# Optimization experiments

Hardware: AMD Instinct MI355X
Metric: run time of the kernel (lower is better)

Reference implementation:

```python
import jax, jax.numpy as jnp
import numpy as np

D_MODEL = 256
N_HEADS = 8
N_LEVELS = 4
N_POINTS = 4
SHAPES = np.array([[64, 64], [32, 32], [16, 16], [8, 8]], dtype=np.int32)


def setup_inputs() -> dict:
    key = jax.random.key(0)
    ks = jax.random.split(key, 10)
    Lq = int((SHAPES[:, 0] * SHAPES[:, 1]).sum())  # 5440
    N, d = 8, D_MODEL
    noff = N_HEADS * N_LEVELS * N_POINTS * 2
    nw = N_HEADS * N_LEVELS * N_POINTS
    s = 1.0 / np.sqrt(d).astype(np.float32)
    inp = {
        'query': jax.random.normal(ks[0], (N, Lq, d), jnp.float32),
        'reference_points': jax.random.uniform(ks[1], (N, Lq, N_LEVELS, 2), jnp.float32),
        'spatial_shapes': jnp.asarray(SHAPES),
        'level_start_index': jnp.asarray(np.concatenate([[0], np.cumsum(SHAPES[:, 0] * SHAPES[:, 1])[:-1]]).astype(np.int32)),
        'W_value': jax.random.normal(ks[2], (d, d), jnp.float32) * s,
        'b_value': jnp.zeros((d,), jnp.float32),
        'W_off': jax.random.normal(ks[3], (d, noff), jnp.float32) * 0.01,
        'b_off': jax.random.uniform(ks[4], (noff,), jnp.float32, minval=-0.5, maxval=0.5),
        'W_attn': jax.random.normal(ks[5], (d, nw), jnp.float32) * s,
        'b_attn': jnp.zeros((nw,), jnp.float32),
        'W_out': jax.random.normal(ks[6], (d, d), jnp.float32) * s,
        'b_out': jnp.zeros((d,), jnp.float32),
    }
    return inp


def _bilinear_sample(val_l, loc_l, H, W):
    # val_l: [N, h, H*W, dh] flattened level feature map
    # loc_l: [N, Lq, h, P, 2] normalized (x, y) in [0, 1]
    # grid_sample semantics, align_corners=False, zero padding
    N, h, HW, dh = val_l.shape
    Lq, P = loc_l.shape[1], loc_l.shape[3]
    x = loc_l[..., 0] * W - 0.5
    y = loc_l[..., 1] * H - 0.5
    x0 = jnp.floor(x)
    y0 = jnp.floor(y)
    wx = (x - x0)[..., None]  # [N, Lq, h, P, 1]
    wy = (y - y0)[..., None]
    x0i = x0.astype(jnp.int32)
    y0i = y0.astype(jnp.int32)

    def gather(yi, xi):
        valid = (xi >= 0) & (xi < W) & (yi >= 0) & (yi < H)  # [N, Lq, h, P]
        idx = jnp.clip(yi, 0, H - 1) * W + jnp.clip(xi, 0, W - 1)
        idx = idx.transpose(0, 2, 1, 3).reshape(N, h, Lq * P)  # [N, h, Lq*P]
        g = jnp.take_along_axis(val_l, jnp.broadcast_to(idx[..., None], (N, h, Lq * P, dh)), axis=2)
        g = g.reshape(N, h, Lq, P, dh)
        mask = valid.transpose(0, 2, 1, 3)[..., None].astype(val_l.dtype)
        return g * mask

    v00 = gather(y0i, x0i)
    v01 = gather(y0i, x0i + 1)
    v10 = gather(y0i + 1, x0i)
    v11 = gather(y0i + 1, x0i + 1)
    wxt = wx.transpose(0, 2, 1, 3, 4)  # [N, h, Lq, P, 1]
    wyt = wy.transpose(0, 2, 1, 3, 4)
    return (v00 * (1 - wxt) * (1 - wyt) + v01 * wxt * (1 - wyt)
            + v10 * (1 - wxt) * wyt + v11 * wxt * wyt)  # [N, h, Lq, P, dh]


def reference(query, reference_points, spatial_shapes, level_start_index,
              W_value, b_value, W_off, b_off, W_attn, b_attn, W_out, b_out):
    shapes = np.asarray(spatial_shapes)  # static level shapes
    N, Lq, d = query.shape
    h, L, P = N_HEADS, N_LEVELS, N_POINTS
    dh = d // h

    v = query @ W_value + b_value  # value_proj (source reassigns query = value_proj(query))
    off = (v @ W_off + b_off).reshape(N, Lq, h, L, P, 2)
    aw = jax.nn.softmax((v @ W_attn + b_attn).reshape(N, Lq, h, L * P), axis=-1)
    aw = aw.reshape(N, Lq, h, L, P)

    # offset_normalizer = [W_l, H_l]
    norm = jnp.asarray(np.stack([shapes[:, 1], shapes[:, 0]], -1), dtype=v.dtype)  # [L, 2]
    loc = reference_points[:, :, None, :, None, :] + off / norm[None, None, None, :, None, :]

    val = v.reshape(N, Lq, h, dh).transpose(0, 2, 1, 3)  # [N, h, Lv, dh]
    out = jnp.zeros((N, h, Lq, dh), v.dtype)
    start = 0
    for l in range(L):
        H, W = int(shapes[l, 0]), int(shapes[l, 1])
        val_l = val[:, :, start:start + H * W]
        sampled = _bilinear_sample(val_l, loc[:, :, :, l], H, W)  # [N, h, Lq, P, dh]
        w_l = aw[:, :, :, l].transpose(0, 2, 1, 3)[..., None]  # [N, h, Lq, P, 1]
        out = out + (sampled * w_l).sum(axis=3)
        start += H * W

    out = out.transpose(0, 2, 1, 3).reshape(N, Lq, d)
    return out @ W_out + b_out
```

## Files before the change

### kernel.cpp

```cpp
#include <hip/hip_runtime.h>
#include <hip/hip_bf16.h>
#include <cstdint>
#include <cstddef>

#define NB 8
#define LQ 5440
#define MROWS (NB * LQ)

typedef __attribute__((ext_vector_type(8))) _Float16       f16x8;
typedef __attribute__((ext_vector_type(4))) float          f32x4;
typedef __attribute__((ext_vector_type(8))) unsigned short ushort8_t;

__device__ __forceinline__ unsigned short f2h(float f) {
    _Float16 h = (_Float16)f;
    unsigned short u;
    __builtin_memcpy(&u, &h, 2);
    return u;
}
__device__ __forceinline__ float h2f(unsigned short u) {
    _Float16 h;
    __builtin_memcpy(&h, &u, 2);
    return (float)h;
}

__global__ __launch_bounds__(256) void prep_weights(
    const float* __restrict__ Wv, const float* __restrict__ Woff,
    const float* __restrict__ Wat, const float* __restrict__ Wo,
    unsigned short* __restrict__ WvT, unsigned short* __restrict__ WoaT,
    unsigned short* __restrict__ WoT)
{
    const int id = blockIdx.x * 256 + threadIdx.x;
    if (id < 65536) {
        const int n = id >> 8, k = id & 255;
        WvT[id] = f2h(Wv[k * 256 + n]);
    } else if (id < 65536 + 98304) {
        const int p = id - 65536;
        const int n = p >> 8, k = p & 255;
        WoaT[p] = (n < 256) ? f2h(Woff[k * 256 + n])
                            : f2h(Wat[k * 128 + (n - 256)]);
    } else {
        const int p = id - (65536 + 98304);
        const int n = p >> 8, k = p & 255;
        WoT[p] = f2h(Wo[k * 256 + n]);
    }
}

#define LDT 40

template<bool A_FP32, bool F16_OUT>
__global__ __launch_bounds__(256) void gemm_mfma(
    const void* __restrict__ Ap, const unsigned short* __restrict__ Bt,
    const float* __restrict__ bias0, const float* __restrict__ bias1,
    void* __restrict__ C0, void* __restrict__ C1,
    int cs0, int cs1, int split)
{
    __shared__ unsigned short As[128 * LDT];
    __shared__ unsigned short Bs[128 * LDT];

    const int bm = blockIdx.y * 128;
    const int bn = blockIdx.x * 128;
    const int t    = threadIdx.x;
    const int lane = t & 63;
    const int wid  = t >> 6;
    const int wm   = (wid >> 1) * 64;
    const int wn   = (wid & 1) * 64;
    const int c    = lane & 15;
    const int qq   = lane >> 4;

    const int tr = t >> 1;
    const int kh = (t & 1) * 16;

    f32x4 acc[4][4];
#pragma unroll
    for (int i = 0; i < 4; ++i)
#pragma unroll
        for (int j = 0; j < 4; ++j)
            acc[i][j] = (f32x4){0.f, 0.f, 0.f, 0.f};

    for (int k0 = 0; k0 < 256; k0 += 32) {
        if (A_FP32) {
            const float4* Af = reinterpret_cast<const float4*>(
                (const float*)Ap + (size_t)(bm + tr) * 256 + k0 + kh);
            const float4 a0 = Af[0], a1 = Af[1], a2 = Af[2], a3 = Af[3];
            ushort8_t u0, u1;
            u0[0]=f2h(a0.x); u0[1]=f2h(a0.y); u0[2]=f2h(a0.z); u0[3]=f2h(a0.w);
            u0[4]=f2h(a1.x); u0[5]=f2h(a1.y); u0[6]=f2h(a1.z); u0[7]=f2h(a1.w);
            u1[0]=f2h(a2.x); u1[1]=f2h(a2.y); u1[2]=f2h(a2.z); u1[3]=f2h(a2.w);
            u1[4]=f2h(a3.x); u1[5]=f2h(a3.y); u1[6]=f2h(a3.z); u1[7]=f2h(a3.w);
            *reinterpret_cast<ushort8_t*>(&As[tr * LDT + kh])     = u0;
            *reinterpret_cast<ushort8_t*>(&As[tr * LDT + kh + 8]) = u1;
        } else {
            const ushort8_t* Ab = reinterpret_cast<const ushort8_t*>(
                (const unsigned short*)Ap + (size_t)(bm + tr) * 256 + k0 + kh);
            *reinterpret_cast<ushort8_t*>(&As[tr * LDT + kh])     = Ab[0];
            *reinterpret_cast<ushort8_t*>(&As[tr * LDT + kh + 8]) = Ab[1];
        }
        {
            const ushort8_t* Bb = reinterpret_cast<const ushort8_t*>(
                Bt + (size_t)(bn + tr) * 256 + k0 + kh);
            *reinterpret_cast<ushort8_t*>(&Bs[tr * LDT + kh])     = Bb[0];
            *reinterpret_cast<ushort8_t*>(&Bs[tr * LDT + kh + 8]) = Bb[1];
        }
        __syncthreads();

        f16x8 af[4], bfr[4];
#pragma unroll
        for (int i = 0; i < 4; ++i)
            af[i] = *reinterpret_cast<const f16x8*>(
                &As[(wm + i * 16 + c) * LDT + qq * 8]);
#pragma unroll
        for (int j = 0; j < 4; ++j)
            bfr[j] = *reinterpret_cast<const f16x8*>(
                &Bs[(wn + j * 16 + c) * LDT + qq * 8]);
#pragma unroll
        for (int i = 0; i < 4; ++i)
#pragma unroll
            for (int j = 0; j < 4; ++j)
                acc[i][j] = __builtin_amdgcn_mfma_f32_16x16x32_f16(
                    af[i], bfr[j], acc[i][j], 0, 0, 0);
        __syncthreads();
    }

#pragma unroll
    for (int j = 0; j < 4; ++j) {
        const int col    = bn + wn + j * 16 + c;
        const bool second = col >= split;
        const int ccol   = second ? col - split : col;
        const float bv   = second ? bias1[ccol] : bias0[ccol];
#pragma unroll
        for (int i = 0; i < 4; ++i) {
#pragma unroll
            for (int r = 0; r < 4; ++r) {
                const int row = bm + wm + i * 16 + qq * 4 + r;
                const float v0 = acc[i][j][r] + bv;
                if (F16_OUT) {
                    const float v1 = __shfl_xor(v0, 1);
                    if ((lane & 1) == 0) {
                        const unsigned int packed =
                            (unsigned int)f2h(v0) | ((unsigned int)f2h(v1) << 16);
                        unsigned short* Cb = (unsigned short*)(second ? C1 : C0);
                        const int cs = second ? cs1 : cs0;
                        *reinterpret_cast<unsigned int*>(
                            Cb + (size_t)row * cs + ccol) = packed;
                    }
                } else {
                    float* Cf = (float*)C0;
                    Cf[(size_t)row * cs0 + col] = v0;
                }
            }
        }
    }
}

__global__ __launch_bounds__(256) void sample_kernel(
    const unsigned short* __restrict__ v16,
    const unsigned short* __restrict__ off16,
    const unsigned short* __restrict__ attn16,
    const float* __restrict__ refpts,
    unsigned short* __restrict__ pre16)
{
    const int lane = threadIdx.x & 63;
    const int wv   = threadIdx.x >> 6;
    const int row  = blockIdx.x * 4 + wv;
    const int n    = row / LQ;

    __shared__ uint4 swi[4][264];

    const ushort4 o4 = reinterpret_cast<const ushort4*>(off16)[(size_t)row * 64 + lane];
    const unsigned int lg = reinterpret_cast<const unsigned int*>(attn16)[(size_t)row * 64 + lane];
    const float l0 = h2f((unsigned short)(lg & 0xffff));
    const float l1 = h2f((unsigned short)(lg >> 16));

    const int h   = lane >> 3;
    const int k   = lane & 7;
    const int j0  = 2 * k;
    const int lev = k >> 1;
    const float rx = refpts[(size_t)row * 8 + lev * 2 + 0];
    const float ry = refpts[(size_t)row * 8 + lev * 2 + 1];

    float m = fmaxf(l0, l1);
    m = fmaxf(m, __shfl_xor(m, 1));
    m = fmaxf(m, __shfl_xor(m, 2));
    m = fmaxf(m, __shfl_xor(m, 4));
    const float e0 = __expf(l0 - m);
    const float e1 = __expf(l1 - m);
    float s = e0 + e1;
    s += __shfl_xor(s, 1);
    s += __shfl_xor(s, 2);
    s += __shfl_xor(s, 4);
    const float inv = 1.f / s;

    const int  W     = 64 >> lev;
    const int  start = (lev == 0) ? 0 : (lev == 1) ? 4096 : (lev == 2) ? 5120 : 5376;
    const float rs   = 0.015625f * (float)(1 << lev);

#pragma unroll
    for (int pp = 0; pp < 2; ++pp) {
        const float lx = rx + h2f(pp ? o4.z : o4.x) * rs;
        const float ly = ry + h2f(pp ? o4.w : o4.y) * rs;
        const float wgt = (pp ? e1 : e0) * inv;

        const float x = lx * (float)W - 0.5f;
        const float y = ly * (float)W - 0.5f;
        const float fx = floorf(x), fy = floorf(y);
        const int xi = (int)fx, yi = (int)fy;
        const float wx = x - fx, wy = y - fy;

        const int x0 = min(max(xi, 0), W - 1);
        const int x1 = min(max(xi + 1, 0), W - 1);
        const int y0 = min(max(yi, 0), W - 1);
        const int y1 = min(max(yi + 1, 0), W - 1);
        const float vx0 = (xi >= 0 && xi < W)         ? (1.f - wx) : 0.f;
        const float vx1 = (xi + 1 >= 0 && xi + 1 < W) ? wx         : 0.f;
        const float vy0 = (yi >= 0 && yi < W)         ? (1.f - wy) : 0.f;
        const float vy1 = (yi + 1 >= 0 && yi + 1 < W) ? wy         : 0.f;

        const int hb  = h * 64;
        const unsigned int b00 = (unsigned int)((start + y0 * W + x0) * 512 + hb);
        const unsigned int b01 = (unsigned int)((start + y0 * W + x1) * 512 + hb);
        const unsigned int b10 = (unsigned int)((start + y1 * W + x0) * 512 + hb);
        const unsigned int b11 = (unsigned int)((start + y1 * W + x1) * 512 + hb);

        const int jj = j0 + pp;
        uint4 c0, c1;
        c0.x = __float_as_uint(wgt * vy0 * vx0);
        c0.y = __float_as_uint(wgt * vy0 * vx1);
        c0.z = b00; c0.w = b01;
        c1.x = __float_as_uint(wgt * vy1 * vx0);
        c1.y = __float_as_uint(wgt * vy1 * vx1);
        c1.z = b10; c1.w = b11;
        swi[wv][h * 33 + jj * 2 + 0] = c0;
        swi[wv][h * 33 + jj * 2 + 1] = c1;
    }
    __syncthreads();

    const int cp = (lane >> 2) & 1;
    const int cg = lane & 3;
    const unsigned int koff = cg * 16;

    const int nu = __builtin_amdgcn_readfirstlane(n);
    const char* vn = reinterpret_cast<const char*>(v16) + (size_t)nu * (LQ * 512);
    const uint4* wib = &swi[wv][h * 33 + cp];

    float acc[8];
#pragma unroll
    for (int i = 0; i < 8; ++i) acc[i] = 0.f;

    uint4 wiA = wib[0];
    uint4 wiB = wib[2];
    ushort8_t vaA = *reinterpret_cast<const ushort8_t*>(vn + (wiA.z + koff));
    ushort8_t vbA = *reinterpret_cast<const ushort8_t*>(vn + (wiA.w + koff));

#pragma unroll
    for (int j = 0; j < 16; ++j) {
        ushort8_t vaB, vbB;
        if (j < 15) {
            vaB = *reinterpret_cast<const ushort8_t*>(vn + (wiB.z + koff));
            vbB = *reinterpret_cast<const ushort8_t*>(vn + (wiB.w + koff));
        }
        uint4 wiC;
        if (j < 14) wiC = wib[2 * (j + 2)];

        const float wa = __uint_as_float(wiA.x);
        const float wb = __uint_as_float(wiA.y);
#pragma unroll
        for (int i = 0; i < 8; ++i)
            acc[i] = fmaf(h2f(vaA[i]), wa, acc[i]);
#pragma unroll
        for (int i = 0; i < 8; ++i)
            acc[i] = fmaf(h2f(vbA[i]), wb, acc[i]);

        wiA = wiB; wiB = wiC; vaA = vaB; vbA = vbB;
    }

#pragma unroll
    for (int i = 0; i < 8; ++i)
        acc[i] += __shfl_xor(acc[i], 4);

    if (cp == 0) {
        ushort8_t st;
#pragma unroll
        for (int i = 0; i < 8; ++i) st[i] = f2h(acc[i]);
        *reinterpret_cast<ushort8_t*>(
            pre16 + (size_t)row * 256 + h * 32 + cg * 8) = st;
    }
}

extern "C" void kernel_launch(void* const* d_in, const int* in_sizes, int n_in,
                              void* d_out, int out_size, void* d_ws, size_t ws_size,
                              hipStream_t stream)
{
    const float* query   = (const float*)d_in[0];
    const float* refpts  = (const float*)d_in[1];
    const float* W_value = (const float*)d_in[4];
    const float* b_value = (const float*)d_in[5];
    const float* W_off   = (const float*)d_in[6];
    const float* b_off   = (const float*)d_in[7];
    const float* W_attn  = (const float*)d_in[8];
    const float* b_attn  = (const float*)d_in[9];
    const float* W_out   = (const float*)d_in[10];
    const float* b_out   = (const float*)d_in[11];
    float* out = (float*)d_out;

    unsigned short* ws_v16   = (unsigned short*)d_ws;
    unsigned short* ws_off16 = ws_v16   + (size_t)MROWS * 256;
    unsigned short* ws_at16  = ws_off16 + (size_t)MROWS * 256;
    unsigned short* ws_pre16 = ws_at16  + (size_t)MROWS * 128;
    unsigned short* ws_wvT   = ws_pre16 + (size_t)MROWS * 256;
    unsigned short* ws_woaT  = ws_wvT   + 65536;
    unsigned short* ws_woT   = ws_woaT  + 98304;

    prep_weights<<<dim3(896), 256, 0, stream>>>(
        W_value, W_off, W_attn, W_out, ws_wvT, ws_woaT, ws_woT);

    gemm_mfma<true, true><<<dim3(2, 340), 256, 0, stream>>>(
        query, ws_wvT, b_value, b_value, ws_v16, ws_v16, 256, 256, 1 << 30);

    gemm_mfma<false, true><<<dim3(3, 340), 256, 0, stream>>>(
        ws_v16, ws_woaT, b_off, b_attn, ws_off16, ws_at16, 256, 128, 256);

    sample_kernel<<<dim3(MROWS / 4), 256, 0, stream>>>(
        ws_v16, ws_off16, ws_at16, refpts, ws_pre16);

    gemm_mfma<false, false><<<dim3(2, 340), 256, 0, stream>>>(
        ws_pre16, ws_woT, b_out, b_out, out, out, 256, 256, 1 << 30);
}
```

Baseline: 143.7 us.

## Fold value projection into offset/attn weights and fuse front GEMMs

Precomputes combined weights W_value·[W_off|W_attn] and the matching fused bias, so that a single front GEMM reads the fp32 query once and writes v, offsets and attention logits together. This removes the second large GEMM pass that re-read v16. The sample kernel also gets a block-index swizzle across batches, a padded shared-memory index layout and a deeper prefetch pipeline for gathers. The trade-offs are extra small setup kernels and a different fp16 rounding path for offsets.

```diff
diff --git a/kernel.cpp b/kernel.cpp
--- a/kernel.cpp
+++ b/kernel.cpp
@@ -26,22 +26,57 @@
 __global__ __launch_bounds__(256) void prep_weights(
     const float* __restrict__ Wv, const float* __restrict__ Woff,
     const float* __restrict__ Wat, const float* __restrict__ Wo,
-    unsigned short* __restrict__ WvT, unsigned short* __restrict__ WoaT,
+    unsigned short* __restrict__ bigBt,
+    unsigned short* __restrict__ Wv16n,
+    unsigned short* __restrict__ WoaT,
     unsigned short* __restrict__ WoT)
 {
     const int id = blockIdx.x * 256 + threadIdx.x;
     if (id < 65536) {
         const int n = id >> 8, k = id & 255;
-        WvT[id] = f2h(Wv[k * 256 + n]);
-    } else if (id < 65536 + 98304) {
+        bigBt[id] = f2h(Wv[k * 256 + n]);
+    } else if (id < 131072) {
         const int p = id - 65536;
+        Wv16n[p] = f2h(Wv[p]);
+    } else if (id < 131072 + 98304) {
+        const int p = id - 131072;
         const int n = p >> 8, k = p & 255;
         WoaT[p] = (n < 256) ? f2h(Woff[k * 256 + n])
                             : f2h(Wat[k * 128 + (n - 256)]);
     } else {
-        const int p = id - (65536 + 98304);
+        const int p = id - (131072 + 98304);
         const int n = p >> 8, k = p & 255;
         WoT[p] = f2h(Wo[k * 256 + n]);
+    }
+}
+
+__global__ __launch_bounds__(256) void combine_bias(
+    const float* __restrict__ b_value, const float* __restrict__ Woff,
+    const float* __restrict__ Wat, const float* __restrict__ b_off,
+    const float* __restrict__ b_attn,
+    float* __restrict__ fbias, float* __restrict__ zb)
+{
+    const int b = blockIdx.x;
+    const int t = threadIdx.x;
+    if (b < 256) {
+        if (t == 0) fbias[b] = b_value[b];
+        return;
+    }
+    if (b >= 640) {
+        const int i = (b - 640) * 256 + t;
+        if (i < 384) zb[i] = 0.f;
+        return;
+    }
+    const int n = b - 256;
+    float p = b_value[t] * ((n < 256) ? Woff[t * 256 + n]
+                                      : Wat[t * 128 + (n - 256)]);
+    for (int o = 32; o >= 1; o >>= 1) p += __shfl_xor(p, o);
+    __shared__ float red[4];
+    if ((t & 63) == 0) red[t >> 6] = p;
+    __syncthreads();
+    if (t == 0) {
+        float s = red[0] + red[1] + red[2] + red[3];
+        fbias[b] = s + ((n < 256) ? b_off[n] : b_attn[n - 256]);
     }
 }
 
@@ -152,6 +187,99 @@
     }
 }
 
+__global__ __launch_bounds__(256) void gemm_front(
+    const float* __restrict__ Ap, const unsigned short* __restrict__ Bt,
+    const float* __restrict__ fbias,
+    unsigned short* __restrict__ v16, unsigned short* __restrict__ off16,
+    unsigned short* __restrict__ at16)
+{
+    __shared__ unsigned short As[128 * LDT];
+    __shared__ unsigned short Bs[128 * LDT];
+
+    const int bm = blockIdx.y * 128;
+    const int bn = blockIdx.x * 128;
+    const int t    = threadIdx.x;
+    const int lane = t & 63;
+    const int wid  = t >> 6;
+    const int wm   = (wid >> 1) * 64;
+    const int wn   = (wid & 1) * 64;
+    const int c    = lane & 15;
+    const int qq   = lane >> 4;
+
+    const int tr = t >> 1;
+    const int kh = (t & 1) * 16;
+
+    f32x4 acc[4][4];
+#pragma unroll
+    for (int i = 0; i < 4; ++i)
+#pragma unroll
+        for (int j = 0; j < 4; ++j)
+            acc[i][j] = (f32x4){0.f, 0.f, 0.f, 0.f};
+
+    for (int k0 = 0; k0 < 256; k0 += 32) {
+        {
+            const float4* Af = reinterpret_cast<const float4*>(
+                Ap + (size_t)(bm + tr) * 256 + k0 + kh);
+            const float4 a0 = Af[0], a1 = Af[1], a2 = Af[2], a3 = Af[3];
+            ushort8_t u0, u1;
+            u0[0]=f2h(a0.x); u0[1]=f2h(a0.y); u0[2]=f2h(a0.z); u0[3]=f2h(a0.w);
+            u0[4]=f2h(a1.x); u0[5]=f2h(a1.y); u0[6]=f2h(a1.z); u0[7]=f2h(a1.w);
+            u1[0]=f2h(a2.x); u1[1]=f2h(a2.y); u1[2]=f2h(a2.z); u1[3]=f2h(a2.w);
+            u1[4]=f2h(a3.x); u1[5]=f2h(a3.y); u1[6]=f2h(a3.z); u1[7]=f2h(a3.w);
+            *reinterpret_cast<ushort8_t*>(&As[tr * LDT + kh])     = u0;
+            *reinterpret_cast<ushort8_t*>(&As[tr * LDT + kh + 8]) = u1;
+        }
+        {
+            const ushort8_t* Bb = reinterpret_cast<const ushort8_t*>(
+                Bt + (size_t)(bn + tr) * 256 + k0 + kh);
+            *reinterpret_cast<ushort8_t*>(&Bs[tr * LDT + kh])     = Bb[0];
+            *reinterpret_cast<ushort8_t*>(&Bs[tr * LDT + kh + 8]) = Bb[1];
+        }
+        __syncthreads();
+
+        f16x8 af[4], bfr[4];
+#pragma unroll
+        for (int i = 0; i < 4; ++i)
+            af[i] = *reinterpret_cast<const f16x8*>(
+                &As[(wm + i * 16 + c) * LDT + qq * 8]);
+#pragma unroll
+        for (int j = 0; j < 4; ++j)
+            bfr[j] = *reinterpret_cast<const f16x8*>(
+                &Bs[(wn + j * 16 + c) * LDT + qq * 8]);
+#pragma unroll
+        for (int i = 0; i < 4; ++i)
+#pragma unroll
+            for (int j = 0; j < 4; ++j)
+                acc[i][j] = __builtin_amdgcn_mfma_f32_16x16x32_f16(
+                    af[i], bfr[j], acc[i][j], 0, 0, 0);
+        __syncthreads();
+    }
+
+#pragma unroll
+    for (int j = 0; j < 4; ++j) {
+        const int col  = bn + wn + j * 16 + c;
+        const float bv = fbias[col];
+#pragma unroll
+        for (int i = 0; i < 4; ++i) {
+#pragma unroll
+            for (int r = 0; r < 4; ++r) {
+                const int row = bm + wm + i * 16 + qq * 4 + r;
+                const float v0 = acc[i][j][r] + bv;
+                const float v1 = __shfl_xor(v0, 1);
+                if ((lane & 1) == 0) {
+                    const unsigned int packed =
+                        (unsigned int)f2h(v0) | ((unsigned int)f2h(v1) << 16);
+                    unsigned short* dst;
+                    if (col < 256)      dst = v16   + (size_t)row * 256 + col;
+                    else if (col < 512) dst = off16 + (size_t)row * 256 + (col - 256);
+                    else                dst = at16  + (size_t)row * 128 + (col - 512);
+                    *reinterpret_cast<unsigned int*>(dst) = packed;
+                }
+            }
+        }
+    }
+}
+
 __global__ __launch_bounds__(256) void sample_kernel(
     const unsigned short* __restrict__ v16,
     const unsigned short* __restrict__ off16,
@@ -161,10 +289,11 @@
 {
     const int lane = threadIdx.x & 63;
     const int wv   = threadIdx.x >> 6;
-    const int row  = blockIdx.x * 4 + wv;
+    const int bid  = (blockIdx.x & 7) * 1360 + (blockIdx.x >> 3);
+    const int row  = bid * 4 + wv;
     const int n    = row / LQ;
 
-    __shared__ uint4 swi[4][264];
+    __shared__ uint4 swi[4][328];
 
     const ushort4 o4 = reinterpret_cast<const ushort4*>(off16)[(size_t)row * 64 + lane];
     const unsigned int lg = reinterpret_cast<const unsigned int*>(attn16)[(size_t)row * 64 + lane];
@@ -173,7 +302,6 @@
 
     const int h   = lane >> 3;
     const int k   = lane & 7;
-    const int j0  = 2 * k;
     const int lev = k >> 1;
     const float rx = refpts[(size_t)row * 8 + lev * 2 + 0];
     const float ry = refpts[(size_t)row * 8 + lev * 2 + 1];
@@ -221,7 +349,6 @@
         const unsigned int b10 = (unsigned int)((start + y1 * W + x0) * 512 + hb);
         const unsigned int b11 = (unsigned int)((start + y1 * W + x1) * 512 + hb);
 
-        const int jj = j0 + pp;
         uint4 c0, c1;
         c0.x = __float_as_uint(wgt * vy0 * vx0);
         c0.y = __float_as_uint(wgt * vy0 * vx1);
@@ -229,8 +356,9 @@
         c1.x = __float_as_uint(wgt * vy1 * vx0);
         c1.y = __float_as_uint(wgt * vy1 * vx1);
         c1.z = b10; c1.w = b11;
-        swi[wv][h * 33 + jj * 2 + 0] = c0;
-        swi[wv][h * 33 + jj * 2 + 1] = c1;
+        const int base = h * 41 + 5 * k + 2 * pp;
+        swi[wv][base + 0] = c0;
+        swi[wv][base + 1] = c1;
     }
     __syncthreads();
 
@@ -240,38 +368,42 @@
 
     const int nu = __builtin_amdgcn_readfirstlane(n);
     const char* vn = reinterpret_cast<const char*>(v16) + (size_t)nu * (LQ * 512);
-    const uint4* wib = &swi[wv][h * 33 + cp];
+    const uint4* wib = &swi[wv][h * 41 + cp];
+
+#define OFS(j) (2 * (j) + ((j) >> 1))
+#define GLD(o) (*reinterpret_cast<const ushort8_t*>(vn + ((o) + koff)))
 
     float acc[8];
 #pragma unroll
     for (int i = 0; i < 8; ++i) acc[i] = 0.f;
 
-    uint4 wiA = wib[0];
-    uint4 wiB = wib[2];
-    ushort8_t vaA = *reinterpret_cast<const ushort8_t*>(vn + (wiA.z + koff));
-    ushort8_t vbA = *reinterpret_cast<const ushort8_t*>(vn + (wiA.w + koff));
+    uint4 wi0 = wib[OFS(0)];
+    uint4 wi1 = wib[OFS(1)];
+    uint4 wi2 = wib[OFS(2)];
+    uint4 wi3 = wi2;
+    ushort8_t va0 = GLD(wi0.z), vb0 = GLD(wi0.w);
+    ushort8_t va1 = GLD(wi1.z), vb1 = GLD(wi1.w);
+    ushort8_t va2 = va1,        vb2 = vb1;
 
 #pragma unroll
     for (int j = 0; j < 16; ++j) {
-        ushort8_t vaB, vbB;
-        if (j < 15) {
-            vaB = *reinterpret_cast<const ushort8_t*>(vn + (wiB.z + koff));
-            vbB = *reinterpret_cast<const ushort8_t*>(vn + (wiB.w + koff));
-        }
-        uint4 wiC;
-        if (j < 14) wiC = wib[2 * (j + 2)];
-
-        const float wa = __uint_as_float(wiA.x);
-        const float wb = __uint_as_float(wiA.y);
+        if (j <= 13) { va2 = GLD(wi2.z); vb2 = GLD(wi2.w); }
+        if (j <= 12) wi3 = wib[OFS(j + 3)];
+
+        const float wa = __uint_as_float(wi0.x);
+        const float wb = __uint_as_float(wi0.y);
 #pragma unroll
         for (int i = 0; i < 8; ++i)
-            acc[i] = fmaf(h2f(vaA[i]), wa, acc[i]);
+            acc[i] = fmaf(h2f(va0[i]), wa, acc[i]);
 #pragma unroll
         for (int i = 0; i < 8; ++i)
-            acc[i] = fmaf(h2f(vbA[i]), wb, acc[i]);
-
-        wiA = wiB; wiB = wiC; vaA = vaB; vbA = vbB;
-    }
+            acc[i] = fmaf(h2f(vb0[i]), wb, acc[i]);
+
+        wi0 = wi1; wi1 = wi2; wi2 = wi3;
+        va0 = va1; va1 = va2; vb0 = vb1; vb1 = vb2;
+    }
+#undef OFS
+#undef GLD
 
 #pragma unroll
     for (int i = 0; i < 8; ++i)
@@ -306,18 +438,25 @@
     unsigned short* ws_off16 = ws_v16   + (size_t)MROWS * 256;
     unsigned short* ws_at16  = ws_off16 + (size_t)MROWS * 256;
     unsigned short* ws_pre16 = ws_at16  + (size_t)MROWS * 128;
-    unsigned short* ws_wvT   = ws_pre16 + (size_t)MROWS * 256;
-    unsigned short* ws_woaT  = ws_wvT   + 65536;
+    unsigned short* ws_bigBt = ws_pre16 + (size_t)MROWS * 256;
+    unsigned short* ws_wv16n = ws_bigBt + 640 * 256;
+    unsigned short* ws_woaT  = ws_wv16n + 65536;
     unsigned short* ws_woT   = ws_woaT  + 98304;
-
-    prep_weights<<<dim3(896), 256, 0, stream>>>(
-        W_value, W_off, W_attn, W_out, ws_wvT, ws_woaT, ws_woT);
-
-    gemm_mfma<true, true><<<dim3(2, 340), 256, 0, stream>>>(
-        query, ws_wvT, b_value, b_value, ws_v16, ws_v16, 256, 256, 1 << 30);
-
-    gemm_mfma<false, true><<<dim3(3, 340), 256, 0, stream>>>(
-        ws_v16, ws_woaT, b_off, b_attn, ws_off16, ws_at16, 256, 128, 256);
+    float*          ws_fbias = (float*)(ws_woT + 65536);
+    float*          ws_zb    = ws_fbias + 640;
+
+    prep_weights<<<dim3(1152), 256, 0, stream>>>(
+        W_value, W_off, W_attn, W_out, ws_bigBt, ws_wv16n, ws_woaT, ws_woT);
+
+    combine_bias<<<dim3(642), 256, 0, stream>>>(
+        b_value, W_off, W_attn, b_off, b_attn, ws_fbias, ws_zb);
+
+    gemm_mfma<false, true><<<dim3(2, 3), 256, 0, stream>>>(
+        ws_woaT, ws_wv16n, ws_zb, ws_zb,
+        ws_bigBt + 65536, ws_bigBt + 65536, 256, 256, 1 << 30);
+
+    gemm_front<<<dim3(5, 340), 256, 0, stream>>>(
+        query, ws_bigBt, ws_fbias, ws_v16, ws_off16, ws_at16);
 
     sample_kernel<<<dim3(MROWS / 4), 256, 0, stream>>>(
         ws_v16, ws_off16, ws_at16, refpts, ws_pre16);
```

Result: slower. 165.0 us (+14.8%).
